# Performance work log

Measured on AMD Instinct MI355X. Metric: run time of the kernel, lower is better.

The kernel has to match this reference:

```python
import jax, jax.numpy as jnp
import numpy as np

N_GRAPH_NODES = 100000  # size of g.ndata['centrality']
N_GRAPH_EDGES = 3200000


def setup_inputs() -> dict:
    key = jax.random.key(0)
    k1, k2, k3, k4 = jax.random.split(key, 4)
    n_node, n_path, l_path = 100000, 32, 8
    paths = jax.random.randint(k1, (n_node, n_path, l_path), 0, N_GRAPH_NODES, dtype=jnp.int32)
    edge_ids = jax.random.randint(k2, (n_node, n_path, l_path - 1), 0, N_GRAPH_EDGES, dtype=jnp.int32)
    rand_lens = jax.random.randint(k3, (n_node, n_path), 0, l_path, dtype=jnp.int32)
    centrality = jax.random.uniform(k4, (N_GRAPH_NODES,), dtype=jnp.float32)
    return {"paths": paths, "edge_ids": edge_ids, "rand_lens": rand_lens,
            "centrality": centrality, "k_path": 8}


def reference(paths, edge_ids, rand_lens, centrality, k_path):
    # paths: [n_node, n_path, l_path] node ids; edge_ids: [n_node, n_path, l_path-1]
    n_node, n_path, l_path = paths.shape
    n_graph = centrality.shape[0]

    # meta_mask[r, j] = (j > r)  (strict upper triangle); paths[mask] = -1
    pos = jnp.arange(l_path, dtype=rand_lens.dtype)  # [l_path]
    masked_paths = jnp.where(pos > rand_lens[..., None], jnp.int32(-1), paths)

    # centrality padded with a trailing zero so id -1 (-> index n_graph) scores 0
    cent_pad = jnp.concatenate([centrality, jnp.zeros((1,), centrality.dtype)])
    gather_idx = jnp.where(masked_paths < 0, n_graph, masked_paths)
    scores = jnp.sum(cent_pad[gather_idx], axis=-1)  # [n_node, n_path]

    # top-k paths per start node by summed centrality
    _, topk_idx = jax.lax.top_k(scores, k_path)  # [n_node, k_path]
    paths_sel = jnp.take_along_axis(masked_paths, topk_idx[:, :, None], axis=1)   # [n_node, k_path, l_path]
    edge_ids_sel = jnp.take_along_axis(edge_ids, topk_idx[:, :, None], axis=1)    # [n_node, k_path, l_path-1]
    return paths_sel, edge_ids_sel
```

## Files before the change

kernel.cpp:

```cpp
#include <hip/hip_runtime.h>


#define N_NODE   100000
#define N_PATH   32
#define L_PATH   8
#define K_PATH   8

typedef int   v4i __attribute__((ext_vector_type(4)));
typedef float v4f __attribute__((ext_vector_type(4)));

__global__ __launch_bounds__(256) void path_sampling_kernel(
    const int*   __restrict__ paths,
    const int*   __restrict__ edge_ids,
    const int*   __restrict__ rand_lens,
    const float* __restrict__ centrality,
    int*         __restrict__ out_paths,
    int*         __restrict__ out_edges)
{
    __shared__ float ssc[4][32];
    __shared__ int   wsrc[4][8];

    const int t    = threadIdx.x;
    const int wv   = t >> 6;
    const int lane = t & 63;
    const int half = lane >> 5;
    const int p    = lane & 31;
    const int node = blockIdx.x * 4 + wv;

    const size_t row = (size_t)node * N_PATH + p;

    v4i mp4 = ((const v4i*)paths)[row * 2 + half];
    int len = rand_lens[row];

    int mp[4] = {mp4.x, mp4.y, mp4.z, mp4.w};

    const int jb = half * 4;
    float c[4];
    #pragma unroll
    for (int k = 0; k < 4; ++k) {
        if (jb + k > len) mp[k] = -1;
        c[k] = (mp[k] < 0) ? 0.0f : centrality[mp[k]];
    }

    const float ps    = (c[0] + c[1]) + (c[2] + c[3]);
    const float other = __shfl_xor(ps, 32);
    const float s     = ps + other;

    if (!half) ssc[wv][p] = s;
    v4f sc[8];
    #pragma unroll
    for (int i = 0; i < 8; ++i) sc[i] = ((const v4f*)ssc[wv])[i];

    const unsigned ltm = (1u << p) - 1u;
    int rank = 0;
    #pragma unroll
    for (int j = 0; j < 32; ++j) {
        const float sj = sc[j >> 2][j & 3];
        rank += (sj > s) || ((sj == s) && ((ltm >> j) & 1u));
    }

    if (rank < K_PATH) {
        const size_t obase = (size_t)node * K_PATH + rank;
        v4i m = {mp[0], mp[1], mp[2], mp[3]};
        ((v4i*)out_paths)[obase * 2 + half] = m;
        if (!half) wsrc[wv][rank] = p;
    }

    const int* ebase = edge_ids + (size_t)node * (N_PATH * (L_PATH - 1));
    int*       edst  = out_edges + (size_t)node * (K_PATH * (L_PATH - 1));
    if (lane < 56) {
        const int r    = lane / 7;
        const int col  = lane - r * 7;
        const int srow = wsrc[wv][r];
        edst[lane] = ebase[srow * 7 + col];
    }
}

extern "C" void kernel_launch(void* const* d_in, const int* in_sizes, int n_in,
                              void* d_out, int out_size, void* d_ws, size_t ws_size,
                              hipStream_t stream) {
    const int*   paths      = (const int*)  d_in[0];
    const int*   edge_ids   = (const int*)  d_in[1];
    const int*   rand_lens  = (const int*)  d_in[2];
    const float* centrality = (const float*)d_in[3];

    int* out_paths = (int*)d_out;
    int* out_edges = out_paths + (size_t)N_NODE * K_PATH * L_PATH;

    const int nodes_per_block = 4;
    const int grid = N_NODE / nodes_per_block;

    path_sampling_kernel<<<grid, 256, 0, stream>>>(
        paths, edge_ids, rand_lens, centrality, out_paths, out_edges);
}
```

Measured before the change: 78.29 us.

## Process node chunks per wave with two-node interleave and prefetch of next pair

Each wavefront now handles a chunk of 14 nodes, processing two nodes per iteration and prefetching the next pair's path rows and lengths while computing the current pair. The grid shrinks accordingly, which amortizes launch and block overhead and exposes more memory-level parallelism per wave. The trade-off is far fewer blocks (about 1786), which may underfill the GPU, plus higher register pressure. There are also LDS reuse hazards, because ssc and wsrc are rewritten across iterations without a barrier, although within one wavefront this is likely safe.

```diff
diff --git a/kernel.cpp b/kernel.cpp
--- a/kernel.cpp
+++ b/kernel.cpp
@@ -5,6 +5,7 @@
 #define N_PATH   32
 #define L_PATH   8
 #define K_PATH   8
+#define CHUNK    14
 
 typedef int   v4i __attribute__((ext_vector_type(4)));
 typedef float v4f __attribute__((ext_vector_type(4)));
@@ -17,62 +18,106 @@
     int*         __restrict__ out_paths,
     int*         __restrict__ out_edges)
 {
-    __shared__ float ssc[4][32];
-    __shared__ int   wsrc[4][8];
+    __shared__ float ssc[4][2][32];
+    __shared__ int   wsrc[4][2][8];
 
     const int t    = threadIdx.x;
     const int wv   = t >> 6;
     const int lane = t & 63;
     const int half = lane >> 5;
     const int p    = lane & 31;
-    const int node = blockIdx.x * 4 + wv;
+    const int gw   = blockIdx.x * 4 + wv;
+    const int base = gw * CHUNK;
 
-    const size_t row = (size_t)node * N_PATH + p;
+    const v4i* P4 = (const v4i*)paths;
 
-    v4i mp4 = ((const v4i*)paths)[row * 2 + half];
-    int len = rand_lens[row];
-
-    int mp[4] = {mp4.x, mp4.y, mp4.z, mp4.w};
-
-    const int jb = half * 4;
-    float c[4];
-    #pragma unroll
-    for (int k = 0; k < 4; ++k) {
-        if (jb + k > len) mp[k] = -1;
-        c[k] = (mp[k] < 0) ? 0.0f : centrality[mp[k]];
+    v4i a, b;
+    int la = 0, lb = 0;
+    if (base < N_NODE) {
+        const size_t r0 = (size_t)base * N_PATH + p;
+        a  = P4[r0 * 2 + half];
+        b  = P4[(r0 + N_PATH) * 2 + half];
+        la = rand_lens[r0];
+        lb = rand_lens[r0 + N_PATH];
     }
 
-    const float ps    = (c[0] + c[1]) + (c[2] + c[3]);
-    const float other = __shfl_xor(ps, 32);
-    const float s     = ps + other;
+    for (int i = 0; i < CHUNK / 2; ++i) {
+        const int n0 = base + 2 * i;
+        if (n0 >= N_NODE) return;
+        const int n1 = n0 + 1;
 
-    if (!half) ssc[wv][p] = s;
-    v4f sc[8];
-    #pragma unroll
-    for (int i = 0; i < 8; ++i) sc[i] = ((const v4f*)ssc[wv])[i];
+        v4i ca4 = a, cb4 = b;
+        const int lena = la, lenb = lb;
 
-    const unsigned ltm = (1u << p) - 1u;
-    int rank = 0;
-    #pragma unroll
-    for (int j = 0; j < 32; ++j) {
-        const float sj = sc[j >> 2][j & 3];
-        rank += (sj > s) || ((sj == s) && ((ltm >> j) & 1u));
-    }
+        const int nn = n0 + 2;
+        if (i + 1 < CHUNK / 2 && nn < N_NODE) {
+            const size_t rn = (size_t)nn * N_PATH + p;
+            a  = P4[rn * 2 + half];
+            b  = P4[(rn + N_PATH) * 2 + half];
+            la = rand_lens[rn];
+            lb = rand_lens[rn + N_PATH];
+        }
 
-    if (rank < K_PATH) {
-        const size_t obase = (size_t)node * K_PATH + rank;
-        v4i m = {mp[0], mp[1], mp[2], mp[3]};
-        ((v4i*)out_paths)[obase * 2 + half] = m;
-        if (!half) wsrc[wv][rank] = p;
-    }
+        const int jb = half * 4;
+        int ma[4] = {ca4.x, ca4.y, ca4.z, ca4.w};
+        int mb[4] = {cb4.x, cb4.y, cb4.z, cb4.w};
+        #pragma unroll
+        for (int k = 0; k < 4; ++k) { if (jb + k > lena) ma[k] = -1; }
+        #pragma unroll
+        for (int k = 0; k < 4; ++k) { if (jb + k > lenb) mb[k] = -1; }
 
-    const int* ebase = edge_ids + (size_t)node * (N_PATH * (L_PATH - 1));
-    int*       edst  = out_edges + (size_t)node * (K_PATH * (L_PATH - 1));
-    if (lane < 56) {
-        const int r    = lane / 7;
-        const int col  = lane - r * 7;
-        const int srow = wsrc[wv][r];
-        edst[lane] = ebase[srow * 7 + col];
+        float ca[4], cb[4];
+        #pragma unroll
+        for (int k = 0; k < 4; ++k) ca[k] = (ma[k] < 0) ? 0.0f : centrality[ma[k]];
+        #pragma unroll
+        for (int k = 0; k < 4; ++k) cb[k] = (mb[k] < 0) ? 0.0f : centrality[mb[k]];
+
+        const float psA = (ca[0] + ca[1]) + (ca[2] + ca[3]);
+        const float psB = (cb[0] + cb[1]) + (cb[2] + cb[3]);
+        const float sA  = psA + __shfl_xor(psA, 32);
+        const float sB  = psB + __shfl_xor(psB, 32);
+
+        if (!half) { ssc[wv][0][p] = sA; ssc[wv][1][p] = sB; }
+
+        const unsigned ltm = (1u << p) - 1u;
+        int rkA = 0, rkB = 0;
+        #pragma unroll
+        for (int q = 0; q < 8; ++q) {
+            const v4f qa = ((const v4f*)ssc[wv][0])[q];
+            const v4f qb = ((const v4f*)ssc[wv][1])[q];
+            #pragma unroll
+            for (int e = 0; e < 4; ++e) {
+                const int j = q * 4 + e;
+                rkA += (qa[e] > sA) || ((qa[e] == sA) && ((ltm >> j) & 1u));
+                rkB += (qb[e] > sB) || ((qb[e] == sB) && ((ltm >> j) & 1u));
+            }
+        }
+
+        if (rkA < K_PATH) {
+            const size_t obase = (size_t)n0 * K_PATH + rkA;
+            v4i m = {ma[0], ma[1], ma[2], ma[3]};
+            ((v4i*)out_paths)[obase * 2 + half] = m;
+            if (!half) wsrc[wv][0][rkA] = p;
+        }
+        if (rkB < K_PATH) {
+            const size_t obase = (size_t)n1 * K_PATH + rkB;
+            v4i m = {mb[0], mb[1], mb[2], mb[3]};
+            ((v4i*)out_paths)[obase * 2 + half] = m;
+            if (!half) wsrc[wv][1][rkB] = p;
+        }
+
+        if (lane < 56) {
+            const int r    = lane / 7;
+            const int col  = lane - r * 7;
+            const int* e0  = edge_ids + (size_t)n0 * (N_PATH * (L_PATH - 1));
+            const int* e1  = edge_ids + (size_t)n1 * (N_PATH * (L_PATH - 1));
+            int* d0 = out_edges + (size_t)n0 * (K_PATH * (L_PATH - 1));
+            int* d1 = out_edges + (size_t)n1 * (K_PATH * (L_PATH - 1));
+            const int s0 = wsrc[wv][0][r];
+            const int s1 = wsrc[wv][1][r];
+            d0[lane] = e0[s0 * 7 + col];
+            d1[lane] = e1[s1 * 7 + col];
+        }
     }
 }
 
@@ -87,8 +132,8 @@
     int* out_paths = (int*)d_out;
     int* out_edges = out_paths + (size_t)N_NODE * K_PATH * L_PATH;
 
-    const int nodes_per_block = 4;
-    const int grid = N_NODE / nodes_per_block;
+    const int nodes_per_block = 4 * CHUNK;
+    const int grid = (N_NODE + nodes_per_block - 1) / nodes_per_block;
 
     path_sampling_kernel<<<grid, 256, 0, stream>>>(
         paths, edge_ids, rand_lens, centrality, out_paths, out_edges);
```

Result: slower. 109.3 us (+39.7%).
